# Optimization experiments

Hardware: AMD Instinct MI355X
Metric: run time of the kernel (lower is better)

Reference implementation:

```python
import jax, jax.numpy as jnp
import numpy as np

N_NODES = 100000
N_EDGES = 2000000
IN_C = 64
OUT_C = 64
K = 27
G = 4


def setup_inputs() -> dict:
    key = jax.random.key(0)
    k1, k2, k3, k4, k5, k6 = jax.random.split(key, 6)
    inp = {
        "input": jax.random.normal(k1, (N_NODES, IN_C), dtype=jnp.float32),
        "i": jax.random.randint(k2, (N_EDGES,), 0, N_NODES),
        "j": jax.random.randint(k3, (N_EDGES,), 0, N_NODES),
        "k": jax.random.randint(k4, (N_EDGES,), 0, K),
        "n": N_NODES,
        "weight": jax.random.normal(k5, (IN_C, OUT_C // G, K), dtype=jnp.float32) * 0.1,
        "bias": jax.random.normal(k6, (OUT_C,), dtype=jnp.float32) * 0.1,
    }
    return inp


def reference(input, i, j, k, n, weight, bias):
    # weight: [in_c, out_c//g, K] -> w: [K, g, in_c//g, out_c//g]
    w = weight.reshape(G, IN_C // G, OUT_C // G, K).transpose(3, 0, 1, 2)
    x3 = input.reshape(input.shape[0], G, IN_C // G)  # [n, g, c]
    # Transform every node by every kernel-position weight once (n*K small GEMMs)
    # instead of materializing a per-edge [E,g,c,d] weight gather.
    x_all = jnp.einsum('ngc,kgcd->nkgd', x3, w)  # [n, K, g, d]
    msgs = x_all[j, k]                            # [E, g, d] gather per edge
    out = jax.ops.segment_sum(msgs, i, num_segments=n)  # scatter-add to dst nodes
    out = out.reshape(-1, OUT_C) + bias
    return out
```

## Files before the change

kernel.cpp:

```cpp
#include <hip/hip_runtime.h>
#include <hip/hip_bf16.h>


#define KPOS 27
#define WPACK_UINTS (KPOS * 512)
#define SCAN_NB 256

typedef unsigned u32x4 __attribute__((ext_vector_type(4)));

__device__ __forceinline__ unsigned packbf(float a, float b) {
    unsigned ua = (unsigned)__bfloat16_as_ushort(__float2bfloat16(a));
    unsigned ub = (unsigned)__bfloat16_as_ushort(__float2bfloat16(b));
    return ua | (ub << 16);
}

#define DOT2(A, X, W) asm("v_dot2_f32_bf16 %0, %1, %2, %0" : "+v"(A) : "v"(X), "v"(W))

__global__ void init_out_kernel(float* __restrict__ out, const float* __restrict__ bias, int total) {
    int idx = blockIdx.x * blockDim.x + threadIdx.x;
    if (idx < total) out[idx] = bias[idx & 63];
}
__global__ void edge_kernel_rawW(const float* __restrict__ input, const int* __restrict__ ei,
                                 const int* __restrict__ ej, const int* __restrict__ ek,
                                 const float* __restrict__ weight, float* __restrict__ out, int n_edges) {
    const int lane = threadIdx.x & 63;
    const int g16 = lane & 48;
    const int d = lane & 15;
    int wave = (blockIdx.x * blockDim.x + threadIdx.x) >> 6;
    int n_waves = (gridDim.x * blockDim.x) >> 6;
    for (int e = wave; e < n_edges; e += n_waves) {
        int ie = ei[e], je = ej[e], ke = ek[e];
        float x = input[je * 64 + lane];
        float acc = 0.0f;
        #pragma unroll
        for (int c = 0; c < 16; ++c)
            acc += __shfl(x, g16 + c, 64) * weight[(g16 + c) * 432 + d * 27 + ke];
        atomicAdd(out + ie * 64 + lane, acc);
    }
}

__global__ void prep_kernel(const float* __restrict__ input, const float* __restrict__ weight,
                            const float* __restrict__ bias, float* __restrict__ out,
                            unsigned* __restrict__ xb, unsigned* __restrict__ wp,
                            int* __restrict__ cnt, int n_nodes, int nquads, int nout4) {
    int t = blockIdx.x * blockDim.x + threadIdx.x;
    if (t < n_nodes) cnt[t] = 0;
    if (t < WPACK_UINTS) {
        int k  = t >> 9;
        int r  = t & 511;
        int q  = r >> 8;
        int r2 = r & 255;
        int gc = r2 >> 2;
        int m  = r2 & 3;
        int g = gc >> 4, d = gc & 15;
        int c = (q * 4 + m) * 2;
        int ic = g * 16 + c;
        float f0 = weight[ic * 432 + d * 27 + k];
        float f1 = weight[(ic + 1) * 432 + d * 27 + k];
        wp[t] = packbf(f0, f1);
    }
    if (t < nquads) {
        const float4* in4 = (const float4*)input;
        float4 a = in4[2 * t], b = in4[2 * t + 1];
        uint4 o;
        o.x = packbf(a.x, a.y);
        o.y = packbf(a.z, a.w);
        o.z = packbf(b.x, b.y);
        o.w = packbf(b.z, b.w);
        ((uint4*)xb)[t] = o;
    }
    if (t < nout4) {
        ((float4*)out)[t] = ((const float4*)bias)[t & 15];
    }
}

__global__ void rank_kernel(const int* __restrict__ ei, int* __restrict__ cnt,
                            unsigned short* __restrict__ rank, int n_edges) {
    int e = blockIdx.x * blockDim.x + threadIdx.x;
    if (e < n_edges)
        rank[e] = (unsigned short)atomicAdd(&cnt[ei[e]], 1);
}

__global__ void scanA_kernel(const int* __restrict__ cnt, int* __restrict__ partial,
                             int n, int chunk) {
    __shared__ int red[256];
    int b = blockIdx.x;
    int lo = b * chunk, hi = min(lo + chunk, n);
    int s = 0;
    for (int v = lo + threadIdx.x; v < hi; v += 256) s += cnt[v];
    red[threadIdx.x] = s;
    __syncthreads();
    for (int d = 128; d > 0; d >>= 1) {
        if (threadIdx.x < d) red[threadIdx.x] += red[threadIdx.x + d];
        __syncthreads();
    }
    if (threadIdx.x == 0) partial[b] = red[0];
}

__global__ void scanB_kernel(int* __restrict__ partial, int* __restrict__ off, int n) {
    __shared__ int sums[SCAN_NB];
    int t = threadIdx.x;
    sums[t] = partial[t];
    __syncthreads();
    for (int d = 1; d < SCAN_NB; d <<= 1) {
        int val = (t >= d) ? sums[t - d] : 0;
        __syncthreads();
        sums[t] += val;
        __syncthreads();
    }
    partial[t] = (t == 0) ? 0 : sums[t - 1];
    if (t == SCAN_NB - 1) off[n] = sums[t];
}

__global__ void scanC_kernel(const int* __restrict__ cnt, const int* __restrict__ partial,
                             int* __restrict__ off, int n, int chunk) {
    __shared__ int excl[256];
    int b = blockIdx.x;
    int lo = b * chunk, hi = min(lo + chunk, n);
    int per = (chunk + 255) >> 8;
    int tlo = lo + threadIdx.x * per;
    int thi = min(tlo + per, hi);
    int s = 0;
    for (int v = tlo; v < thi; ++v) s += cnt[v];
    excl[threadIdx.x] = s;
    __syncthreads();
    for (int d = 1; d < 256; d <<= 1) {
        int val = (threadIdx.x >= d) ? excl[threadIdx.x - d] : 0;
        __syncthreads();
        excl[threadIdx.x] += val;
        __syncthreads();
    }
    int run = partial[b] + ((threadIdx.x == 0) ? 0 : excl[threadIdx.x - 1]);
    for (int v = tlo; v < thi; ++v) { off[v] = run; run += cnt[v]; }
}

__global__ void fill_kernel(const int* __restrict__ ei, const int* __restrict__ ej,
                            const int* __restrict__ ek, const int* __restrict__ off,
                            const unsigned short* __restrict__ rank,
                            uint2* __restrict__ recs, int n_edges) {
    int e = blockIdx.x * blockDim.x + threadIdx.x;
    if (e < n_edges) {
        int ie = ei[e];
        uint2 r;
        r.x = (unsigned)ej[e] | ((unsigned)ek[e] << 17);
        r.y = (unsigned)ie;
        recs[off[ie] + (int)rank[e]] = r;
    }
}

__launch_bounds__(1024, 8)
__global__ void gather_kernel(const unsigned* __restrict__ xb,
                              const uint2* __restrict__ recs,
                              const unsigned* __restrict__ wp,
                              float* __restrict__ out, int n_edges) {
    __shared__ unsigned lds[WPACK_UINTS];
    for (int t = threadIdx.x; t < WPACK_UINTS / 4; t += blockDim.x)
        ((uint4*)lds)[t] = ((const uint4*)wp)[t];
    __syncthreads();

    const int lane = threadIdx.x & 63;
    const int g8   = (lane & 48) >> 1;
    const unsigned* wl = lds + (lane << 2);

    int wid = (blockIdx.x * blockDim.x + threadIdx.x) >> 6;
    int nw  = (gridDim.x * blockDim.x) >> 6;
    int epw = (((n_edges + nw - 1) / nw) + 7) & ~7;
    int e    = wid * epw;
    int eend = min(e + epw, n_edges);
    if (e >= eend) return;

    int  cur = -1;
    float a0l = 0.0f, a0h = 0.0f, a1l = 0.0f, a1h = 0.0f;

#define FLUSH_CHANGE() do {                                                   \
        if (cur >= 0) {                                                       \
            float s_ = (a0l + a0h) + (a1l + a1h);                             \
            atomicAdd(out + (cur << 6) + lane, s_);                           \
            a0l = a0h = a1l = a1h = 0.0f;                                     \
        }                                                                     \
    } while (0)

#define EDGE_BODY(P, AL, AH)                                                \
        do {                                                                \
            unsigned p_ = (P);                                              \
            const u32x4* wr = (const u32x4*)(wl + ((p_ >> 17) << 9));       \
            const u32x4* xr = (const u32x4*)(xb + ((p_ & 0x1FFFFu) << 5) + g8); \
            u32x4 xa = xr[0], xc = xr[1];                                   \
            u32x4 wa = wr[0], wb = wr[64];                                  \
            DOT2(AL, xa[0], wa[0]); DOT2(AH, xa[1], wa[1]);                 \
            DOT2(AL, xa[2], wa[2]); DOT2(AH, xa[3], wa[3]);                 \
            DOT2(AL, xc[0], wb[0]); DOT2(AH, xc[1], wb[1]);                 \
            DOT2(AL, xc[2], wb[2]); DOT2(AH, xc[3], wb[3]);                 \
        } while (0)

    for (; e + 4 <= eend; e += 4) {
        const uint4* rc = (const uint4*)(recs + e);
        uint4 r01 = rc[0], r23 = rc[1];
        const u32x4* x0 = (const u32x4*)(xb + ((r01.x & 0x1FFFFu) << 5) + g8);
        const u32x4* x1 = (const u32x4*)(xb + ((r01.z & 0x1FFFFu) << 5) + g8);
        const u32x4* x2 = (const u32x4*)(xb + ((r23.x & 0x1FFFFu) << 5) + g8);
        const u32x4* x3 = (const u32x4*)(xb + ((r23.z & 0x1FFFFu) << 5) + g8);
        u32x4 xa0 = x0[0], xc0 = x0[1];
        u32x4 xa1 = x1[0], xc1 = x1[1];
        u32x4 xa2 = x2[0], xc2 = x2[1];
        u32x4 xa3 = x3[0], xc3 = x3[1];
        int i0 = __builtin_amdgcn_readfirstlane((int)r01.y);
        int i1 = __builtin_amdgcn_readfirstlane((int)r01.w);
        int i2 = __builtin_amdgcn_readfirstlane((int)r23.y);
        int i3 = __builtin_amdgcn_readfirstlane((int)r23.w);

        if (i0 != cur) { FLUSH_CHANGE(); cur = i0; }
        {
            const u32x4* wr = (const u32x4*)(wl + ((r01.x >> 17) << 9));
            u32x4 wa = wr[0], wb2 = wr[64];
            DOT2(a0l, xa0[0], wa[0]); DOT2(a0h, xa0[1], wa[1]);
            DOT2(a0l, xa0[2], wa[2]); DOT2(a0h, xa0[3], wa[3]);
            DOT2(a0l, xc0[0], wb2[0]); DOT2(a0h, xc0[1], wb2[1]);
            DOT2(a0l, xc0[2], wb2[2]); DOT2(a0h, xc0[3], wb2[3]);
        }
        if (i1 != cur) { FLUSH_CHANGE(); cur = i1; }
        {
            const u32x4* wr = (const u32x4*)(wl + ((r01.z >> 17) << 9));
            u32x4 wa = wr[0], wb2 = wr[64];
            DOT2(a1l, xa1[0], wa[0]); DOT2(a1h, xa1[1], wa[1]);
            DOT2(a1l, xa1[2], wa[2]); DOT2(a1h, xa1[3], wa[3]);
            DOT2(a1l, xc1[0], wb2[0]); DOT2(a1h, xc1[1], wb2[1]);
            DOT2(a1l, xc1[2], wb2[2]); DOT2(a1h, xc1[3], wb2[3]);
        }
        if (i2 != cur) { FLUSH_CHANGE(); cur = i2; }
        {
            const u32x4* wr = (const u32x4*)(wl + ((r23.x >> 17) << 9));
            u32x4 wa = wr[0], wb2 = wr[64];
            DOT2(a0l, xa2[0], wa[0]); DOT2(a0h, xa2[1], wa[1]);
            DOT2(a0l, xa2[2], wa[2]); DOT2(a0h, xa2[3], wa[3]);
            DOT2(a0l, xc2[0], wb2[0]); DOT2(a0h, xc2[1], wb2[1]);
            DOT2(a0l, xc2[2], wb2[2]); DOT2(a0h, xc2[3], wb2[3]);
        }
        if (i3 != cur) { FLUSH_CHANGE(); cur = i3; }
        {
            const u32x4* wr = (const u32x4*)(wl + ((r23.z >> 17) << 9));
            u32x4 wa = wr[0], wb2 = wr[64];
            DOT2(a1l, xa3[0], wa[0]); DOT2(a1h, xa3[1], wa[1]);
            DOT2(a1l, xa3[2], wa[2]); DOT2(a1h, xa3[3], wa[3]);
            DOT2(a1l, xc3[0], wb2[0]); DOT2(a1h, xc3[1], wb2[1]);
            DOT2(a1l, xc3[2], wb2[2]); DOT2(a1h, xc3[3], wb2[3]);
        }
    }

    for (; e < eend; ++e) {
        uint2 r = recs[e];
        int ri = __builtin_amdgcn_readfirstlane((int)r.y);
        if (ri != cur) { FLUSH_CHANGE(); cur = ri; }
        EDGE_BODY(r.x, a0l, a0h);
    }

    FLUSH_CHANGE();
#undef EDGE_BODY
#undef FLUSH_CHANGE
}

static inline size_t al256(size_t x) { return (x + 255) & ~(size_t)255; }

extern "C" void kernel_launch(void* const* d_in, const int* in_sizes, int n_in,
                              void* d_out, int out_size, void* d_ws, size_t ws_size,
                              hipStream_t stream) {
    const float* input  = (const float*)d_in[0];
    const int*   ei     = (const int*)d_in[1];
    const int*   ej     = (const int*)d_in[2];
    const int*   ek     = (const int*)d_in[3];
    const float* weight = (const float*)d_in[5];
    const float* bias   = (const float*)d_in[6];

    const int n_edges = in_sizes[1];
    const int n_nodes = out_size / 64;

    size_t off_o  = 0;
    size_t off_s  = al256((size_t)(n_nodes + 1) * 4);
    size_t cnt_o  = off_o + off_s;
    size_t cnt_s  = al256((size_t)n_nodes * 4);
    size_t par_o  = cnt_o + cnt_s;
    size_t par_s  = al256((size_t)SCAN_NB * 4);
    size_t rank_o = par_o + par_s;
    size_t rank_s = al256((size_t)n_edges * 2);
    size_t rec_o  = rank_o + rank_s;
    size_t rec_s  = al256((size_t)n_edges * 8);
    size_t wp_o   = rec_o + rec_s;
    size_t wp_s   = al256((size_t)WPACK_UINTS * 4);
    size_t xb_o   = wp_o + wp_s;
    size_t xb_s   = al256((size_t)n_nodes * 64 * 2);
    size_t need   = xb_o + xb_s;

    if (ws_size < need) {
        int blocks = (out_size + 255) / 256;
        hipLaunchKernelGGL(init_out_kernel, dim3(blocks), dim3(256), 0, stream,
                           (float*)d_out, bias, out_size);
        hipLaunchKernelGGL(edge_kernel_rawW, dim3(2048), dim3(256), 0, stream,
                           input, ei, ej, ek, weight, (float*)d_out, n_edges);
        return;
    }

    char* ws = (char*)d_ws;
    int*            off  = (int*)(ws + off_o);
    int*            cnt  = (int*)(ws + cnt_o);
    int*            par  = (int*)(ws + par_o);
    unsigned short* rank = (unsigned short*)(ws + rank_o);
    uint2*          recs = (uint2*)(ws + rec_o);
    unsigned*       wp   = (unsigned*)(ws + wp_o);
    unsigned*       xb   = (unsigned*)(ws + xb_o);

    const int eb = (n_edges + 255) / 256;
    const int nquads = n_nodes * 8;
    const int nout4  = n_nodes * 16;
    const int prep_range = max(max(nquads, nout4), max(n_nodes, WPACK_UINTS));
    const int chunk = (n_nodes + SCAN_NB - 1) / SCAN_NB;

    hipLaunchKernelGGL(prep_kernel, dim3((prep_range + 255) / 256), dim3(256), 0, stream,
                       input, weight, bias, (float*)d_out, xb, wp, cnt,
                       n_nodes, nquads, nout4);
    hipLaunchKernelGGL(rank_kernel, dim3(eb), dim3(256), 0, stream, ei, cnt, rank, n_edges);
    hipLaunchKernelGGL(scanA_kernel, dim3(SCAN_NB), dim3(256), 0, stream, cnt, par, n_nodes, chunk);
    hipLaunchKernelGGL(scanB_kernel, dim3(1), dim3(SCAN_NB), 0, stream, par, off, n_nodes);
    hipLaunchKernelGGL(scanC_kernel, dim3(SCAN_NB), dim3(256), 0, stream, cnt, par, off, n_nodes, chunk);
    hipLaunchKernelGGL(fill_kernel, dim3(eb), dim3(256), 0, stream, ei, ej, ek, off, rank, recs, n_edges);

    hipLaunchKernelGGL(gather_kernel, dim3(512), dim3(1024), 0, stream,
                       xb, recs, wp, (float*)d_out, n_edges);
}
```

Measured before the change: 299.7 us.

## Split each wave into two half-waves processing separate edges with two outputs per lane

Restructures the gather kernel so each 64-lane wave handles two edges at once, one per 32-lane half. Each lane now computes two output channels and does twice the weight reads from LDS per edge. Destination changes are tracked per lane with divergent flushes. The goal is to halve the iterations per edge and raise memory-level parallelism. In exchange it brings more divergence, twice the atomics per flush (two per lane), and zeroed padding for tail edges.

```diff
diff --git a/kernel.cpp b/kernel.cpp
--- a/kernel.cpp
+++ b/kernel.cpp
@@ -158,105 +158,74 @@
         ((uint4*)lds)[t] = ((const uint4*)wp)[t];
     __syncthreads();
 
-    const int lane = threadIdx.x & 63;
-    const int g8   = (lane & 48) >> 1;
-    const unsigned* wl = lds + (lane << 2);
+    const int lane  = threadIdx.x & 63;
+    const int half  = lane >> 5;
+    const int g     = (lane >> 3) & 3;
+    const int dp    = lane & 7;
+    const int g8u   = g << 3;
+    const int wbase = ((g << 4) + dp) << 2;
+    const int och   = (g << 4) + dp;
 
     int wid = (blockIdx.x * blockDim.x + threadIdx.x) >> 6;
     int nw  = (gridDim.x * blockDim.x) >> 6;
-    int epw = (((n_edges + nw - 1) / nw) + 7) & ~7;
+    int epw = (((n_edges + nw - 1) / nw) + 3) & ~3;
     int e    = wid * epw;
     int eend = min(e + epw, n_edges);
     if (e >= eend) return;
 
-    int  cur = -1;
-    float a0l = 0.0f, a0h = 0.0f, a1l = 0.0f, a1h = 0.0f;
-
-#define FLUSH_CHANGE() do {                                                   \
-        if (cur >= 0) {                                                       \
-            float s_ = (a0l + a0h) + (a1l + a1h);                             \
-            atomicAdd(out + (cur << 6) + lane, s_);                           \
-            a0l = a0h = a1l = a1h = 0.0f;                                     \
+    const int elast = n_edges - 1;
+    int cur = -1;
+    float a0l = 0.f, a0h = 0.f, a1l = 0.f, a1h = 0.f;
+
+#define FLUSH_LANE() do {                                                     \
+        atomicAdd(out + (cur << 6) + och,     a0l + a0h);                     \
+        atomicAdd(out + (cur << 6) + och + 8, a1l + a1h);                     \
+    } while (0)
+
+#define EDGE_SET(RX, RY, XA, XC) do {                                         \
+        int ri_ = (int)(RY);                                                  \
+        if (__any(ri_ != cur)) {                                              \
+            bool ch_ = (ri_ != cur);                                          \
+            if (ch_) {                                                        \
+                if (cur >= 0) FLUSH_LANE();                                   \
+                cur = ri_;                                                    \
+                a0l = a0h = a1l = a1h = 0.f;                                  \
+            }                                                                 \
+        }                                                                     \
+        {                                                                     \
+            const u32x4* wq_ = (const u32x4*)(lds + (((RX) >> 17) << 9) + wbase); \
+            u32x4 w00 = wq_[0], w01 = wq_[64], w10 = wq_[8], w11 = wq_[72];   \
+            DOT2(a0l, XA[0], w00[0]); DOT2(a0l, XA[1], w00[1]);               \
+            DOT2(a0l, XA[2], w00[2]); DOT2(a0l, XA[3], w00[3]);               \
+            DOT2(a0h, XC[0], w01[0]); DOT2(a0h, XC[1], w01[1]);               \
+            DOT2(a0h, XC[2], w01[2]); DOT2(a0h, XC[3], w01[3]);               \
+            DOT2(a1l, XA[0], w10[0]); DOT2(a1l, XA[1], w10[1]);               \
+            DOT2(a1l, XA[2], w10[2]); DOT2(a1l, XA[3], w10[3]);               \
+            DOT2(a1h, XC[0], w11[0]); DOT2(a1h, XC[1], w11[1]);               \
+            DOT2(a1h, XC[2], w11[2]); DOT2(a1h, XC[3], w11[3]);               \
         }                                                                     \
     } while (0)
 
-#define EDGE_BODY(P, AL, AH)                                                \
-        do {                                                                \
-            unsigned p_ = (P);                                              \
-            const u32x4* wr = (const u32x4*)(wl + ((p_ >> 17) << 9));       \
-            const u32x4* xr = (const u32x4*)(xb + ((p_ & 0x1FFFFu) << 5) + g8); \
-            u32x4 xa = xr[0], xc = xr[1];                                   \
-            u32x4 wa = wr[0], wb = wr[64];                                  \
-            DOT2(AL, xa[0], wa[0]); DOT2(AH, xa[1], wa[1]);                 \
-            DOT2(AL, xa[2], wa[2]); DOT2(AH, xa[3], wa[3]);                 \
-            DOT2(AL, xc[0], wb[0]); DOT2(AH, xc[1], wb[1]);                 \
-            DOT2(AL, xc[2], wb[2]); DOT2(AH, xc[3], wb[3]);                 \
-        } while (0)
-
-    for (; e + 4 <= eend; e += 4) {
-        const uint4* rc = (const uint4*)(recs + e);
-        uint4 r01 = rc[0], r23 = rc[1];
-        const u32x4* x0 = (const u32x4*)(xb + ((r01.x & 0x1FFFFu) << 5) + g8);
-        const u32x4* x1 = (const u32x4*)(xb + ((r01.z & 0x1FFFFu) << 5) + g8);
-        const u32x4* x2 = (const u32x4*)(xb + ((r23.x & 0x1FFFFu) << 5) + g8);
-        const u32x4* x3 = (const u32x4*)(xb + ((r23.z & 0x1FFFFu) << 5) + g8);
-        u32x4 xa0 = x0[0], xc0 = x0[1];
-        u32x4 xa1 = x1[0], xc1 = x1[1];
-        u32x4 xa2 = x2[0], xc2 = x2[1];
-        u32x4 xa3 = x3[0], xc3 = x3[1];
-        int i0 = __builtin_amdgcn_readfirstlane((int)r01.y);
-        int i1 = __builtin_amdgcn_readfirstlane((int)r01.w);
-        int i2 = __builtin_amdgcn_readfirstlane((int)r23.y);
-        int i3 = __builtin_amdgcn_readfirstlane((int)r23.w);
-
-        if (i0 != cur) { FLUSH_CHANGE(); cur = i0; }
-        {
-            const u32x4* wr = (const u32x4*)(wl + ((r01.x >> 17) << 9));
-            u32x4 wa = wr[0], wb2 = wr[64];
-            DOT2(a0l, xa0[0], wa[0]); DOT2(a0h, xa0[1], wa[1]);
-            DOT2(a0l, xa0[2], wa[2]); DOT2(a0h, xa0[3], wa[3]);
-            DOT2(a0l, xc0[0], wb2[0]); DOT2(a0h, xc0[1], wb2[1]);
-            DOT2(a0l, xc0[2], wb2[2]); DOT2(a0h, xc0[3], wb2[3]);
-        }
-        if (i1 != cur) { FLUSH_CHANGE(); cur = i1; }
-        {
-            const u32x4* wr = (const u32x4*)(wl + ((r01.z >> 17) << 9));
-            u32x4 wa = wr[0], wb2 = wr[64];
-            DOT2(a1l, xa1[0], wa[0]); DOT2(a1h, xa1[1], wa[1]);
-            DOT2(a1l, xa1[2], wa[2]); DOT2(a1h, xa1[3], wa[3]);
-            DOT2(a1l, xc1[0], wb2[0]); DOT2(a1h, xc1[1], wb2[1]);
-            DOT2(a1l, xc1[2], wb2[2]); DOT2(a1h, xc1[3], wb2[3]);
-        }
-        if (i2 != cur) { FLUSH_CHANGE(); cur = i2; }
-        {
-            const u32x4* wr = (const u32x4*)(wl + ((r23.x >> 17) << 9));
-            u32x4 wa = wr[0], wb2 = wr[64];
-            DOT2(a0l, xa2[0], wa[0]); DOT2(a0h, xa2[1], wa[1]);
-            DOT2(a0l, xa2[2], wa[2]); DOT2(a0h, xa2[3], wa[3]);
-            DOT2(a0l, xc2[0], wb2[0]); DOT2(a0h, xc2[1], wb2[1]);
-            DOT2(a0l, xc2[2], wb2[2]); DOT2(a0h, xc2[3], wb2[3]);
-        }
-        if (i3 != cur) { FLUSH_CHANGE(); cur = i3; }
-        {
-            const u32x4* wr = (const u32x4*)(wl + ((r23.z >> 17) << 9));
-            u32x4 wa = wr[0], wb2 = wr[64];
-            DOT2(a1l, xa3[0], wa[0]); DOT2(a1h, xa3[1], wa[1]);
-            DOT2(a1l, xa3[2], wa[2]); DOT2(a1h, xa3[3], wa[3]);
-            DOT2(a1l, xc3[0], wb2[0]); DOT2(a1h, xc3[1], wb2[1]);
-            DOT2(a1l, xc3[2], wb2[2]); DOT2(a1h, xc3[3], wb2[3]);
-        }
-    }
-
-    for (; e < eend; ++e) {
-        uint2 r = recs[e];
-        int ri = __builtin_amdgcn_readfirstlane((int)r.y);
-        if (ri != cur) { FLUSH_CHANGE(); cur = ri; }
-        EDGE_BODY(r.x, a0l, a0h);
-    }
-
-    FLUSH_CHANGE();
-#undef EDGE_BODY
-#undef FLUSH_CHANGE
+    for (; e < eend; e += 4) {
+        int i0 = e + half, i1 = e + 2 + half;
+        bool v0 = i0 < eend, v1 = i1 < eend;
+        if (i0 > elast) i0 = elast;
+        if (i1 > elast) i1 = elast;
+        uint2 r0 = recs[i0], r1 = recs[i1];
+        const u32x4* xp0 = (const u32x4*)(xb + ((r0.x & 0x1FFFFu) << 5) + g8u);
+        const u32x4* xp1 = (const u32x4*)(xb + ((r1.x & 0x1FFFFu) << 5) + g8u);
+        u32x4 xa0 = xp0[0], xc0 = xp0[1];
+        u32x4 xa1 = xp1[0], xc1 = xp1[1];
+        if (!v0) { xa0[0]=xa0[1]=xa0[2]=xa0[3]=0u; xc0[0]=xc0[1]=xc0[2]=xc0[3]=0u; }
+        if (!v1) { xa1[0]=xa1[1]=xa1[2]=xa1[3]=0u; xc1[0]=xc1[1]=xc1[2]=xc1[3]=0u; }
+
+        EDGE_SET(r0.x, r0.y, xa0, xc0);
+        EDGE_SET(r1.x, r1.y, xa1, xc1);
+    }
+
+    if (cur >= 0) FLUSH_LANE();
+#undef EDGE_SET
+#undef FLUSH_LANE
 }
 
 static inline size_t al256(size_t x) { return (x + 255) & ~(size_t)255; }
```

Result: no change. 294.2 us (-1.8%).
